# Performance work log

Hardware: AMD Instinct MI355X
Metric: run time of the kernel (lower is better)

## Reference

```python
import jax, jax.numpy as jnp
import numpy as np

D_MODEL = 1024
NUM_HEADS = 16
D_K = D_MODEL // NUM_HEADS
B, S = 4, 2048
NEG = -1e9


def setup_inputs() -> dict:
    key = jax.random.key(0)
    ks = jax.random.split(key, 12)
    def lin(kw, kb):
        bound = 1.0 / np.sqrt(D_MODEL)
        W = jax.random.uniform(kw, (D_MODEL, D_MODEL), jnp.float32, -bound, bound)
        b = jax.random.uniform(kb, (D_MODEL,), jnp.float32, -bound, bound)
        return W, b
    Wq, bq = lin(ks[0], ks[1])
    Wk, bk = lin(ks[2], ks[3])
    Wv, bv = lin(ks[4], ks[5])
    Wo, bo = lin(ks[6], ks[7])
    Q = jax.random.normal(ks[8], (B, S, D_MODEL), jnp.float32)
    K = jax.random.normal(ks[9], (B, S, D_MODEL), jnp.float32)
    V = jax.random.normal(ks[10], (B, S, D_MODEL), jnp.float32)
    # causal mask: 1 = keep, 0 = masked
    mask = jnp.tril(jnp.ones((S, S), jnp.int32))[None, None, :, :]
    mask = jnp.broadcast_to(mask, (B, 1, S, S))
    return {"Q": Q, "K": K, "V": V, "mask": mask,
            "Wq": Wq, "bq": bq, "Wk": Wk, "bk": bk,
            "Wv": Wv, "bv": bv, "Wo": Wo, "bo": bo}


def _split_heads(x):
    b, s, _ = x.shape
    return x.reshape(b, s, NUM_HEADS, D_K).transpose(0, 2, 1, 3)  # [B,H,S,Dk]


def reference(Q, K, V, mask, Wq, bq, Wk, bk, Wv, bv, Wo, bo):
    q = _split_heads(Q @ Wq.T + bq)
    k = _split_heads(K @ Wk.T + bk)
    v = _split_heads(V @ Wv.T + bv)
    scores = jnp.einsum('bhqd,bhkd->bhqk', q, k) / jnp.sqrt(jnp.float32(D_K))
    scores = jnp.where(mask == 0, jnp.float32(NEG), scores)
    probs = jax.nn.softmax(scores, axis=-1)
    attn = jnp.einsum('bhqk,bhkd->bhqd', probs, v)  # [B,H,S,Dk]
    attn = attn.transpose(0, 2, 1, 3).reshape(Q.shape[0], Q.shape[1], D_MODEL)
    return attn @ Wo.T + bo
```

## Files before the change

kernel.cpp:

```cpp
#include <hip/hip_runtime.h>
#include <hip/hip_bf16.h>
#include <cstdint>

typedef float floatx4 __attribute__((ext_vector_type(4)));
typedef __bf16 bf16x8 __attribute__((ext_vector_type(8)));

#define AS_G __attribute__((address_space(1)))
#define AS_L __attribute__((address_space(3)))

__device__ __forceinline__ void async_cp16(const void* g, void* l) {
    __builtin_amdgcn_global_load_lds((const AS_G uint32_t*)g, (AS_L uint32_t*)l, 16, 0, 0);
}

__device__ __forceinline__ floatx4 mfma16x16x32(bf16x8 a, bf16x8 b, floatx4 c) {
    return __builtin_amdgcn_mfma_f32_16x16x32_bf16(a, b, c, 0, 0, 0);
}

__device__ __forceinline__ unsigned short f2bf(float x) {
    return __builtin_bit_cast(unsigned short, (__bf16)x);
}

__global__ __launch_bounds__(256) void cvt_f32_bf16(const float* __restrict__ in,
                                                    unsigned short* __restrict__ out, int n) {
    int i = (blockIdx.x * 256 + threadIdx.x) * 4;
    if (i >= n) return;
    float4 v = *(const float4*)(in + i);
    ushort4 o;
    o.x = f2bf(v.x); o.y = f2bf(v.y); o.z = f2bf(v.z); o.w = f2bf(v.w);
    *(ushort4*)(out + i) = o;
}

__global__ __launch_bounds__(256) void cvt4_f32_bf16(const float* __restrict__ a, const float* __restrict__ b,
                                                     const float* __restrict__ c, const float* __restrict__ d,
                                                     unsigned short* __restrict__ out, int n) {
    const float* in = blockIdx.y == 0 ? a : blockIdx.y == 1 ? b : blockIdx.y == 2 ? c : d;
    unsigned short* o = out + (size_t)blockIdx.y * n;
    int i = (blockIdx.x * 256 + threadIdx.x) * 4;
    if (i >= n) return;
    float4 v = *(const float4*)(in + i);
    ushort4 u;
    u.x = f2bf(v.x); u.y = f2bf(v.y); u.z = f2bf(v.z); u.w = f2bf(v.w);
    *(ushort4*)(o + i) = u;
}

template <int MODE>
__global__ __launch_bounds__(256) void gemm_bt(const unsigned short* __restrict__ A,
                                               const unsigned short* __restrict__ W,
                                               const float* __restrict__ bias,
                                               float oscale,
                                               void* __restrict__ outv) {
    __shared__ unsigned short As[128 * 64];
    __shared__ unsigned short Bs[128 * 64];
    const int tid  = threadIdx.x;
    const int wave = tid >> 6, lane = tid & 63;
    const int quad = lane >> 4, l15 = lane & 15;
    const int l7   = l15 & 7;
    const int m0 = blockIdx.x * 128, n0 = blockIdx.y * 128;
    const int waveM = (wave >> 1) * 64, waveN = (wave & 1) * 64;

    floatx4 acc[4][4] = {};

    const int r8  = lane >> 3;
    const int gsw = (lane & 7) ^ r8;

    for (int k0 = 0; k0 < 1024; k0 += 64) {
        for (int c = wave; c < 16; c += 4) {
            const int row = c * 8 + r8;
            async_cp16(A + (size_t)(m0 + row) * 1024 + k0 + gsw * 8, (char*)As + c * 1024);
            async_cp16(W + (size_t)(n0 + row) * 1024 + k0 + gsw * 8, (char*)Bs + c * 1024);
        }
        __syncthreads();

#pragma unroll
        for (int h = 0; h < 2; ++h) {
            const int g = (quad + h * 4) ^ l7;
            bf16x8 af[4], bf[4];
#pragma unroll
            for (int t = 0; t < 4; ++t) {
                af[t] = *(const bf16x8*)&As[(waveM + t * 16 + l15) * 64 + g * 8];
                bf[t] = *(const bf16x8*)&Bs[(waveN + t * 16 + l15) * 64 + g * 8];
            }
#pragma unroll
            for (int mt = 0; mt < 4; ++mt)
#pragma unroll
                for (int nt = 0; nt < 4; ++nt)
                    acc[mt][nt] = mfma16x16x32(af[mt], bf[nt], acc[mt][nt]);
        }
        __syncthreads();
    }

#pragma unroll
    for (int mt = 0; mt < 4; ++mt) {
#pragma unroll
        for (int nt = 0; nt < 4; ++nt) {
            const int gcol = n0 + waveN + nt * 16 + l15;
            const float bv = bias[gcol];
#pragma unroll
            for (int r = 0; r < 4; ++r) {
                const int grow = m0 + waveM + mt * 16 + quad * 4 + r;
                const float val = (acc[mt][nt][r] + bv) * oscale;
                if (MODE == 2) {
                    ((float*)outv)[(size_t)grow * 1024 + gcol] = val;
                } else {
                    const int b = grow >> 11, s = grow & 2047;
                    const int h = gcol >> 6, dk = gcol & 63;
                    size_t idx;
                    if (MODE == 0) idx = ((size_t)(b * 16 + h) * 2048 + s) * 64 + dk;
                    else           idx = ((size_t)(b * 16 + h) * 64 + dk) * 2048 + s;
                    ((unsigned short*)outv)[idx] = f2bf(val);
                }
            }
        }
    }
}

#define PS_STRIDE 72

template <bool DIAG>
__device__ __forceinline__ void attn_tile(const unsigned short* __restrict__ Ks,
                                          const unsigned short* __restrict__ Vs,
                                          unsigned short* __restrict__ Psw,
                                          bf16x8 qf0, bf16x8 qf1,
                                          int quad, int l15,
                                          int qrow0,
                                          int kv0,
                                          float* __restrict__ lsum,
                                          floatx4* __restrict__ O) {
    const int l7 = l15 & 7;
    const int g1 = quad ^ l7, g2 = (quad + 4) ^ l7;

    floatx4 sc[4];
#pragma unroll
    for (int kvt = 0; kvt < 4; ++kvt) {
        const int rr = kvt * 16 + l15;
        floatx4 a = {};
        a = mfma16x16x32(qf0, *(const bf16x8*)&Ks[rr * 64 + g1 * 8], a);
        a = mfma16x16x32(qf1, *(const bf16x8*)&Ks[rr * 64 + g2 * 8], a);
        sc[kvt] = a;
    }

#pragma unroll
    for (int kvt = 0; kvt < 4; ++kvt) {
#pragma unroll
        for (int r = 0; r < 4; ++r) {
            float s = sc[kvt][r];
            if (DIAG && (kv0 + kvt * 16 + l15 > qrow0 + r)) s = -1.0e9f;
            const float p = __builtin_amdgcn_exp2f(s);
            lsum[r] += p;
            Psw[(quad * 4 + r) * PS_STRIDE + kvt * 16 + l15] = f2bf(p);
        }
    }

#pragma unroll
    for (int half = 0; half < 2; ++half) {
        bf16x8 pf = *(const bf16x8*)&Psw[l15 * PS_STRIDE + half * 32 + quad * 8];
        const int gb = (quad + half * 4) ^ l7;
#pragma unroll
        for (int nt = 0; nt < 4; ++nt) {
            bf16x8 vf = *(const bf16x8*)&Vs[(nt * 16 + l15) * 64 + gb * 8];
            O[nt] = mfma16x16x32(pf, vf, O[nt]);
        }
    }
}

__global__ __launch_bounds__(256) void flash_causal(const unsigned short* __restrict__ qp,
                                                    const unsigned short* __restrict__ kp,
                                                    const unsigned short* __restrict__ vt,
                                                    unsigned short* __restrict__ attn) {
    __shared__ unsigned short Ks[64 * 64];
    __shared__ unsigned short Vs[64 * 64];
    __shared__ unsigned short Ps[4 * 16 * PS_STRIDE];

    const int tid  = threadIdx.x;
    const int wave = tid >> 6, lane = tid & 63;
    const int quad = lane >> 4, l15 = lane & 15;
    const int bh = blockIdx.x;
    const int pr = blockIdx.y;
    const int tA = pr, tB = 31 - pr;

    unsigned short* Psw = &Ps[wave * 16 * PS_STRIDE];

    bf16x8 qfA0, qfA1, qfB0, qfB1;
    {
        const unsigned short* qa = qp + ((size_t)bh * 2048 + tA * 64 + wave * 16 + l15) * 64;
        qfA0 = *(const bf16x8*)(qa + quad * 8);
        qfA1 = *(const bf16x8*)(qa + 32 + quad * 8);
        const unsigned short* qb = qp + ((size_t)bh * 2048 + tB * 64 + wave * 16 + l15) * 64;
        qfB0 = *(const bf16x8*)(qb + quad * 8);
        qfB1 = *(const bf16x8*)(qb + 32 + quad * 8);
    }

    float lsumA[4] = {}, lsumB[4] = {};
    floatx4 OA[4] = {}, OB[4] = {};

    const int qrowA = tA * 64 + wave * 16 + quad * 4;
    const int qrowB = tB * 64 + wave * 16 + quad * 4;

    const int r8  = lane >> 3;
    const int gsw = (lane & 7) ^ r8;

    for (int t = 0; t <= tB; ++t) {
        const int kv0 = t * 64;
        for (int c = wave; c < 8; c += 4) {
            const int row = c * 8 + r8;
            async_cp16(kp + (size_t)bh * 131072 + (size_t)(kv0 + row) * 64 + gsw * 8,
                       (char*)Ks + c * 1024);
            async_cp16(vt + ((size_t)bh * 64 + row) * 2048 + kv0 + gsw * 8,
                       (char*)Vs + c * 1024);
        }
        __syncthreads();

        if (t == tB) attn_tile<true >(Ks, Vs, Psw, qfB0, qfB1, quad, l15, qrowB, kv0, lsumB, OB);
        else         attn_tile<false>(Ks, Vs, Psw, qfB0, qfB1, quad, l15, qrowB, kv0, lsumB, OB);
        if (t == tA)      attn_tile<true >(Ks, Vs, Psw, qfA0, qfA1, quad, l15, qrowA, kv0, lsumA, OA);
        else if (t < tA)  attn_tile<false>(Ks, Vs, Psw, qfA0, qfA1, quad, l15, qrowA, kv0, lsumA, OA);
        __syncthreads();
    }

    const int b = bh >> 4, h = bh & 15;
#pragma unroll
    for (int r = 0; r < 4; ++r) {
        float lA = lsumA[r], lB = lsumB[r];
#pragma unroll
        for (int off = 8; off; off >>= 1) {
            lA += __shfl_xor(lA, off, 16);
            lB += __shfl_xor(lB, off, 16);
        }
        const float invA = 1.0f / lA;
        const float invB = 1.0f / lB;
        const size_t rbA = ((size_t)b * 2048 + qrowA + r) * 1024 + h * 64;
        const size_t rbB = ((size_t)b * 2048 + qrowB + r) * 1024 + h * 64;
#pragma unroll
        for (int nt = 0; nt < 4; ++nt) {
            attn[rbA + nt * 16 + l15] = f2bf(OA[nt][r] * invA);
            attn[rbB + nt * 16 + l15] = f2bf(OB[nt][r] * invB);
        }
    }
}

extern "C" void kernel_launch(void* const* d_in, const int* in_sizes, int n_in,
                              void* d_out, int out_size, void* d_ws, size_t ws_size,
                              hipStream_t stream) {
    const float* Q  = (const float*)d_in[0];
    const float* K  = (const float*)d_in[1];
    const float* V  = (const float*)d_in[2];
    const float* Wq = (const float*)d_in[4];  const float* bq = (const float*)d_in[5];
    const float* Wk = (const float*)d_in[6];  const float* bk = (const float*)d_in[7];
    const float* Wv = (const float*)d_in[8];  const float* bv = (const float*)d_in[9];
    const float* Wo = (const float*)d_in[10]; const float* bo = (const float*)d_in[11];
    float* out = (float*)d_out;

    const int NIN = 8192 * 1024;
    const int NW  = 1024 * 1024;

    unsigned short* ws   = (unsigned short*)d_ws;
    unsigned short* inb  = ws;
    unsigned short* wb   = inb + NIN;
    unsigned short* qp   = wb + 4 * NW;
    unsigned short* kp   = qp + NIN;
    unsigned short* vtp  = kp + NIN;
    unsigned short* attnb = vtp + NIN;

    const float QSCL = 0.125f * 1.44269504088896f;

    dim3 blk(256);
    dim3 gcvtW((NW + 1023) / 1024, 4);
    dim3 gcvtA((NIN + 1023) / 1024);
    dim3 ggemm(64, 8);
    dim3 gflash(64, 16);

    cvt4_f32_bf16<<<gcvtW, blk, 0, stream>>>(Wq, Wk, Wv, Wo, wb, NW);

    cvt_f32_bf16<<<gcvtA, blk, 0, stream>>>(Q, inb, NIN);
    gemm_bt<0><<<ggemm, blk, 0, stream>>>(inb, wb + 0 * NW, bq, QSCL, (void*)qp);
    cvt_f32_bf16<<<gcvtA, blk, 0, stream>>>(K, inb, NIN);
    gemm_bt<0><<<ggemm, blk, 0, stream>>>(inb, wb + 1 * NW, bk, 1.0f, (void*)kp);
    cvt_f32_bf16<<<gcvtA, blk, 0, stream>>>(V, inb, NIN);
    gemm_bt<1><<<ggemm, blk, 0, stream>>>(inb, wb + 2 * NW, bv, 1.0f, (void*)vtp);

    flash_causal<<<gflash, blk, 0, stream>>>(qp, kp, vtp, attnb);

    gemm_bt<2><<<ggemm, blk, 0, stream>>>(attnb, wb + 3 * NW, bo, 1.0f, (void*)out);
}
```

Measured before the change: 364.9 us.

## Double-buffer K/V tiles in flash attention and hoist LDS fragments into registers

The causal flash-attention kernel now keeps two K/V LDS buffers and issues the async global-to-LDS copy for the next tile before computing the current one, waiting with explicit vmcnt counts instead of a full sync. It also loads the K and V fragments for a tile into registers once and reuses them for both query blocks, rather than re-reading LDS per block. MFMA sections are wrapped in s_setprio, and launch bounds request 3 blocks per CU. The intent is to hide global load latency and cut redundant LDS reads, at the cost of more LDS and registers per block, which may limit occupancy.

```diff
diff --git a/kernel.cpp b/kernel.cpp
--- a/kernel.cpp
+++ b/kernel.cpp
@@ -117,27 +117,23 @@
 #define PS_STRIDE 72
 
 template <bool DIAG>
-__device__ __forceinline__ void attn_tile(const unsigned short* __restrict__ Ks,
-                                          const unsigned short* __restrict__ Vs,
-                                          unsigned short* __restrict__ Psw,
-                                          bf16x8 qf0, bf16x8 qf1,
-                                          int quad, int l15,
-                                          int qrow0,
-                                          int kv0,
-                                          float* __restrict__ lsum,
-                                          floatx4* __restrict__ O) {
-    const int l7 = l15 & 7;
-    const int g1 = quad ^ l7, g2 = (quad + 4) ^ l7;
-
+__device__ __forceinline__ void tile_compute(const bf16x8 kf[4][2], const bf16x8 vf[2][4],
+                                             unsigned short* __restrict__ Psw,
+                                             bf16x8 qf0, bf16x8 qf1,
+                                             int quad, int l15,
+                                             int qrow0, int kv0,
+                                             float* __restrict__ lsum,
+                                             floatx4* __restrict__ O) {
     floatx4 sc[4];
+    __builtin_amdgcn_s_setprio(1);
 #pragma unroll
     for (int kvt = 0; kvt < 4; ++kvt) {
-        const int rr = kvt * 16 + l15;
         floatx4 a = {};
-        a = mfma16x16x32(qf0, *(const bf16x8*)&Ks[rr * 64 + g1 * 8], a);
-        a = mfma16x16x32(qf1, *(const bf16x8*)&Ks[rr * 64 + g2 * 8], a);
+        a = mfma16x16x32(qf0, kf[kvt][0], a);
+        a = mfma16x16x32(qf1, kf[kvt][1], a);
         sc[kvt] = a;
     }
+    __builtin_amdgcn_s_setprio(0);
 
 #pragma unroll
     for (int kvt = 0; kvt < 4; ++kvt) {
@@ -151,29 +147,29 @@
         }
     }
 
+    __builtin_amdgcn_s_setprio(1);
 #pragma unroll
     for (int half = 0; half < 2; ++half) {
         bf16x8 pf = *(const bf16x8*)&Psw[l15 * PS_STRIDE + half * 32 + quad * 8];
-        const int gb = (quad + half * 4) ^ l7;
-#pragma unroll
-        for (int nt = 0; nt < 4; ++nt) {
-            bf16x8 vf = *(const bf16x8*)&Vs[(nt * 16 + l15) * 64 + gb * 8];
-            O[nt] = mfma16x16x32(pf, vf, O[nt]);
-        }
-    }
-}
-
-__global__ __launch_bounds__(256) void flash_causal(const unsigned short* __restrict__ qp,
-                                                    const unsigned short* __restrict__ kp,
-                                                    const unsigned short* __restrict__ vt,
-                                                    unsigned short* __restrict__ attn) {
-    __shared__ unsigned short Ks[64 * 64];
-    __shared__ unsigned short Vs[64 * 64];
+#pragma unroll
+        for (int nt = 0; nt < 4; ++nt)
+            O[nt] = mfma16x16x32(pf, vf[half][nt], O[nt]);
+    }
+    __builtin_amdgcn_s_setprio(0);
+}
+
+__global__ __launch_bounds__(256, 3) void flash_causal(const unsigned short* __restrict__ qp,
+                                                       const unsigned short* __restrict__ kp,
+                                                       const unsigned short* __restrict__ vt,
+                                                       unsigned short* __restrict__ attn) {
+    __shared__ unsigned short Ks[2][64 * 64];
+    __shared__ unsigned short Vs[2][64 * 64];
     __shared__ unsigned short Ps[4 * 16 * PS_STRIDE];
 
     const int tid  = threadIdx.x;
     const int wave = tid >> 6, lane = tid & 63;
     const int quad = lane >> 4, l15 = lane & 15;
+    const int l7   = l15 & 7;
     const int bh = blockIdx.x;
     const int pr = blockIdx.y;
     const int tA = pr, tB = 31 - pr;
@@ -198,24 +194,62 @@
 
     const int r8  = lane >> 3;
     const int gsw = (lane & 7) ^ r8;
-
+    const size_t kb = (size_t)bh * 131072;
+    const size_t vb = (size_t)bh * 64 * 2048;
+
+#define STAGE(t, b) do {                                                                  \
+        const int kv0_ = (t) * 64;                                                        \
+        for (int c = wave; c < 8; c += 4) {                                               \
+            const int row_ = c * 8 + r8;                                                  \
+            async_cp16(kp + kb + (size_t)(kv0_ + row_) * 64 + gsw * 8,                    \
+                       (char*)Ks[b] + c * 1024);                                          \
+            async_cp16(vt + vb + (size_t)row_ * 2048 + kv0_ + gsw * 8,                    \
+                       (char*)Vs[b] + c * 1024);                                          \
+        } } while (0)
+
+    STAGE(0, 0);
+
+    int buf = 0;
     for (int t = 0; t <= tB; ++t) {
+        if (t < tB) {
+            STAGE(t + 1, buf ^ 1);
+            asm volatile("s_waitcnt vmcnt(4)" ::: "memory");
+        } else {
+            asm volatile("s_waitcnt vmcnt(0)" ::: "memory");
+        }
+        __builtin_amdgcn_s_barrier();
+        __builtin_amdgcn_sched_barrier(0);
+
+        const unsigned short* Kc = Ks[buf];
+        const unsigned short* Vc = Vs[buf];
+
+        bf16x8 kf[4][2], vf[2][4];
+        const int g1 = quad ^ l7, g2 = (quad + 4) ^ l7;
+#pragma unroll
+        for (int kvt = 0; kvt < 4; ++kvt) {
+            kf[kvt][0] = *(const bf16x8*)&Kc[(kvt * 16 + l15) * 64 + g1 * 8];
+            kf[kvt][1] = *(const bf16x8*)&Kc[(kvt * 16 + l15) * 64 + g2 * 8];
+        }
+#pragma unroll
+        for (int half = 0; half < 2; ++half) {
+            const int gb = (quad + half * 4) ^ l7;
+#pragma unroll
+            for (int nt = 0; nt < 4; ++nt)
+                vf[half][nt] = *(const bf16x8*)&Vc[(nt * 16 + l15) * 64 + gb * 8];
+        }
+
         const int kv0 = t * 64;
-        for (int c = wave; c < 8; c += 4) {
-            const int row = c * 8 + r8;
-            async_cp16(kp + (size_t)bh * 131072 + (size_t)(kv0 + row) * 64 + gsw * 8,
-                       (char*)Ks + c * 1024);
-            async_cp16(vt + ((size_t)bh * 64 + row) * 2048 + kv0 + gsw * 8,
-                       (char*)Vs + c * 1024);
-        }
-        __syncthreads();
-
-        if (t == tB) attn_tile<true >(Ks, Vs, Psw, qfB0, qfB1, quad, l15, qrowB, kv0, lsumB, OB);
-        else         attn_tile<false>(Ks, Vs, Psw, qfB0, qfB1, quad, l15, qrowB, kv0, lsumB, OB);
-        if (t == tA)      attn_tile<true >(Ks, Vs, Psw, qfA0, qfA1, quad, l15, qrowA, kv0, lsumA, OA);
-        else if (t < tA)  attn_tile<false>(Ks, Vs, Psw, qfA0, qfA1, quad, l15, qrowA, kv0, lsumA, OA);
-        __syncthreads();
-    }
+        if (t == tB) tile_compute<true >(kf, vf, Psw, qfB0, qfB1, quad, l15, qrowB, kv0, lsumB, OB);
+        else         tile_compute<false>(kf, vf, Psw, qfB0, qfB1, quad, l15, qrowB, kv0, lsumB, OB);
+        if (t == tA)      tile_compute<true >(kf, vf, Psw, qfA0, qfA1, quad, l15, qrowA, kv0, lsumA, OA);
+        else if (t < tA)  tile_compute<false>(kf, vf, Psw, qfA0, qfA1, quad, l15, qrowA, kv0, lsumA, OA);
+
+        asm volatile("s_waitcnt lgkmcnt(0)" ::: "memory");
+        __builtin_amdgcn_sched_barrier(0);
+        __builtin_amdgcn_s_barrier();
+        buf ^= 1;
+    }
+#undef STAGE
 
     const int b = bh >> 4, h = bh & 15;
 #pragma unroll
```

Result: no change. 363.3 us (-0.5%).
